# Performance work log

Measured on AMD Instinct MI355X. Metric: run time of the kernel, lower is better.

The kernel has to match this reference:

```python
import jax, jax.numpy as jnp
import numpy as np
from jax import lax

B, CIN, H, W = 8, 256, 32, 32
DK, DV, NH = 256, 256, 8
DKH = DK // NH
COUT = 512  # output_dim; conv path has COUT - DV channels
KS, PAD = 3, 1


def setup_inputs() -> dict:
    key = jax.random.key(0)
    ks = jax.random.split(key, 9)
    scale = DKH ** (-0.5)
    return {
        "x": jax.random.normal(ks[0], (B, CIN, H, W), jnp.float32),
        "w_qkv": jax.random.normal(ks[1], (2 * DK + DV, CIN), jnp.float32) * 0.02,
        "b_qkv": jnp.zeros((2 * DK + DV,), jnp.float32),
        "w_attn": jax.random.normal(ks[2], (DV, DV), jnp.float32) * 0.02,
        "b_attn": jnp.zeros((DV,), jnp.float32),
        "w_out": jax.random.normal(ks[3], (COUT - DV, CIN, KS, KS), jnp.float32) * 0.02,
        "b_out": jnp.zeros((COUT - DV,), jnp.float32),
        # original: dkh**-0.5 + torch.rand(2*W-1, dkh)
        "key_rel_w": scale + jax.random.uniform(ks[4], (2 * W - 1, DKH), jnp.float32),
        "key_rel_h": scale + jax.random.uniform(ks[5], (2 * H - 1, DKH), jnp.float32),
    }


def _conv1x1(x, w, b):
    return jnp.einsum("bchw,oc->bohw", x, w) + b[None, :, None, None]


def _rel_to_abs(x):
    # x: [b, nh, L, 2L-1] -> [b, nh, L, L] via pad-reshape-slice trick
    b, nh, L, _ = x.shape
    x = jnp.pad(x, ((0, 0), (0, 0), (0, 0), (0, 1)))            # [b,nh,L,2L]
    flat = x.reshape(b, nh, L * 2 * L)
    flat = jnp.pad(flat, ((0, 0), (0, 0), (0, L - 1)))
    final = flat.reshape(b, nh, L + 1, 2 * L - 1)
    return final[:, :, :L, L - 1:]


def _rel_logits_1d(q5, rel_k, h, w, nh, perm):
    # q5: [b, nh, dkh, h, w]; rel_k: [2w-1, dkh]
    b = q5.shape[0]
    rel = jnp.einsum("bhdxy,md->bhxym", q5, rel_k)               # [b,nh,h,w,2w-1]
    rel = rel.reshape(b, nh * h, w, 2 * w - 1)
    rel = _rel_to_abs(rel)                                        # [b,nh*h,w,w]
    rel = rel.reshape(b, nh, h, w, w)
    rel = jnp.broadcast_to(rel[:, :, :, None], (b, nh, h, h, w, w))
    rel = jnp.transpose(rel, perm)                                # [b,nh,H,W,H,W]
    return rel.reshape(b, nh, h * w, h * w)


def reference(x, w_qkv, b_qkv, w_attn, b_attn, w_out, b_out, key_rel_w, key_rel_h):
    b = x.shape[0]
    hw = H * W
    # parallel conv path (3x3, pad 1)
    conv_out = lax.conv_general_dilated(
        x, w_out, window_strides=(1, 1), padding=((PAD, PAD), (PAD, PAD)),
        dimension_numbers=("NCHW", "OIHW", "NCHW")) + b_out[None, :, None, None]
    # qkv via 1x1 conv
    qkv = _conv1x1(x, w_qkv, b_qkv)
    q, k, v = jnp.split(qkv, [DK, 2 * DK], axis=1)
    q = q.reshape(b, NH, DKH, hw) * (DKH ** (-0.5))
    k = k.reshape(b, NH, DKH, hw)
    v = v.reshape(b, NH, DV // NH, hw)
    logits = jnp.einsum("bhdq,bhdk->bhqk", q, k)                  # [b,nh,HW,HW]
    q5 = q.reshape(b, NH, DKH, H, W)
    w_rel = _rel_logits_1d(q5, key_rel_w, H, W, NH, (0, 1, 2, 4, 3, 5))
    h_rel = _rel_logits_1d(jnp.transpose(q5, (0, 1, 2, 4, 3)), key_rel_h, W, H, NH,
                           (0, 1, 4, 2, 5, 3))
    logits = logits + h_rel + w_rel
    weights = jax.nn.softmax(logits, axis=-1)
    attn = jnp.einsum("bhqk,bhdk->bhdq", weights, v)              # [b,nh,dvh,HW]
    attn = attn.reshape(b, DV, H, W)
    attn = _conv1x1(attn, w_attn, b_attn)
    return jnp.concatenate([conv_out, attn], axis=1)
```

## Files before the change

kernel.cpp:

```cpp
#include <hip/hip_runtime.h>
#include <hip/hip_bf16.h>


typedef __hip_bfloat16 bf16;
using short8 = __attribute__((ext_vector_type(8))) short;
using short4v = __attribute__((ext_vector_type(4))) short;
using f32x4 = __attribute__((ext_vector_type(4))) float;

__device__ __forceinline__ short f2bs(float f) {
  union { bf16 b; short s; } u; u.b = __float2bfloat16(f); return u.s;
}
__device__ __forceinline__ float bs2f(short s) {
  union { unsigned u; float f; } x; x.u = ((unsigned)(unsigned short)s) << 16;
  return x.f;
}

__global__ __launch_bounds__(256) void xpose(
    const float* __restrict__ X, short* __restrict__ xt,
    short* __restrict__ xb2) {
  const int b = blockIdx.x, r = blockIdx.y;
  const int tid = threadIdx.x;
  if (r == 0 || r == 33) {
    short8 z = {};
    short* dst = xt + (((size_t)b * 34 + r) * 34) * 256;
    for (int g = tid; g < 1088; g += 256) *(short8*)(dst + g * 8) = z;
    return;
  }
  __shared__ short xls[32][264];
  {
    const float* src = X + (size_t)b * 256 * 1024 + (r - 1) * 32;
    for (int it = 0; it < 8; ++it) {
      int idx = it * 256 + tid;
      int c = idx >> 3, pq = idx & 7;
      float4 f4 = *(const float4*)(src + (size_t)c * 1024 + pq * 4);
      xls[pq * 4 + 0][c] = f2bs(f4.x);
      xls[pq * 4 + 1][c] = f2bs(f4.y);
      xls[pq * 4 + 2][c] = f2bs(f4.z);
      xls[pq * 4 + 3][c] = f2bs(f4.w);
    }
  }
  __syncthreads();
  {
    short* dst = xt + (((size_t)b * 34 + r) * 34) * 256;
    for (int it = 0; it < 4; ++it) {
      int idx = it * 256 + tid;
      int cc = idx >> 5, co = idx & 31;
      short8 v = *(const short8*)&xls[cc][co * 8];
      *(short8*)(dst + (cc + 1) * 256 + co * 8) = v;
    }
    if (tid < 64) {
      short8 z = {};
      int cce = (tid >> 5) * 33, co = tid & 31;
      *(short8*)(dst + cce * 256 + co * 8) = z;
    }
  }
  {
    short* dst = xb2 + (((size_t)b * 64 + (r - 1) * 2) * 8) * 512;
    for (int it = 0; it < 4; ++it) {
      int g = it * 256 + tid;
      int half = g >> 9, c8 = (g >> 6) & 7, grp = (g >> 4) & 3, pcol = g & 15;
      short8 v = *(const short8*)&xls[half * 16 + pcol][c8 * 32 + grp * 8];
      *(short8*)(dst + ((half * 8 + c8) * 64 + grp * 16 + pcol) * 8) = v;
    }
  }
}

__global__ __launch_bounds__(256) void wpack(
    const float* __restrict__ Wc, short* __restrict__ Wb,
    const float* __restrict__ wq, short* __restrict__ Wq,
    const float* __restrict__ wa, short* __restrict__ Wa) {
  const int bid = blockIdx.x;
  const int tid = threadIdx.x;
  if (bid < 256) {
    __shared__ float ws[2304];
    const float* src = Wc + (size_t)bid * 2304;
    for (int it = 0; it < 9; ++it) ws[it * 256 + tid] = src[it * 256 + tid];
    __syncthreads();
#pragma unroll
    for (int tap = 0; tap < 9; ++tap)
      Wb[tap * 65536 + bid * 256 + tid] = f2bs(ws[tid * 9 + tap]);
  } else if (bid < 1024) {
    int idx = (bid - 256) * 256 + tid;
    Wq[idx] = f2bs(wq[idx]);
  } else {
    int idx = (bid - 1024) * 256 + tid;
    Wa[idx] = f2bs(wa[idx]);
  }
}

__global__ __launch_bounds__(256) void qkv_mfma(
    const short* __restrict__ Wq, const short* __restrict__ xb2,
    const float* __restrict__ bias,
    short* __restrict__ qsb, short* __restrict__ ksb, short* __restrict__ vtb) {
  const int tid = threadIdx.x;
  const int w = tid >> 6, lane = tid & 63;
  const int col = lane & 15, grp = lane >> 4, g8 = grp * 8;
  const int b = blockIdx.z;
  const int p0 = blockIdx.x * 64;
  const int og = blockIdx.y * 128;
  const int ob = og + w * 16;

  const short* wa0 = Wq + (size_t)(ob + col) * 256 + g8;
  const short* wa1 = wa0 + (size_t)64 * 256;
  const short* xpb = xb2 + (((size_t)b * 64 + blockIdx.x * 4) * 8) * 512 + lane * 8;

  f32x4 acc[2][4] = {};
#pragma unroll
  for (int c8 = 0; c8 < 8; ++c8) {
    const int chb = c8 * 32;
    short8 a0 = *(const short8*)(wa0 + chb);
    short8 a1 = *(const short8*)(wa1 + chb);
    short8 b0 = *(const short8*)(xpb + c8 * 512);
    short8 b1 = *(const short8*)(xpb + 4096 + c8 * 512);
    short8 b2 = *(const short8*)(xpb + 8192 + c8 * 512);
    short8 b3 = *(const short8*)(xpb + 12288 + c8 * 512);
    acc[0][0] = __builtin_amdgcn_mfma_f32_16x16x32_bf16(a0, b0, acc[0][0], 0, 0, 0);
    acc[0][1] = __builtin_amdgcn_mfma_f32_16x16x32_bf16(a0, b1, acc[0][1], 0, 0, 0);
    acc[0][2] = __builtin_amdgcn_mfma_f32_16x16x32_bf16(a0, b2, acc[0][2], 0, 0, 0);
    acc[0][3] = __builtin_amdgcn_mfma_f32_16x16x32_bf16(a0, b3, acc[0][3], 0, 0, 0);
    acc[1][0] = __builtin_amdgcn_mfma_f32_16x16x32_bf16(a1, b0, acc[1][0], 0, 0, 0);
    acc[1][1] = __builtin_amdgcn_mfma_f32_16x16x32_bf16(a1, b1, acc[1][1], 0, 0, 0);
    acc[1][2] = __builtin_amdgcn_mfma_f32_16x16x32_bf16(a1, b2, acc[1][2], 0, 0, 0);
    acc[1][3] = __builtin_amdgcn_mfma_f32_16x16x32_bf16(a1, b3, acc[1][3], 0, 0, 0);
  }

  const float qscale = 0.17677669529663687f;
#pragma unroll
  for (int j = 0; j < 2; ++j) {
    const int obase = ob + j * 64 + grp * 4;
    const int sect = obase >> 8;
    const int nh = (obase >> 5) & 7;
    const int d0 = obase & 31;
    const size_t hb = ((size_t)(b * 8 + nh)) * 1024;
    float bv[4];
#pragma unroll
    for (int r = 0; r < 4; ++r) bv[r] = bias[obase + r];
    if (sect == 0) {
#pragma unroll
      for (int pp = 0; pp < 4; ++pp) {
        const int p = p0 + pp * 16 + col;
        short4v o4;
#pragma unroll
        for (int r = 0; r < 4; ++r)
          o4[r] = f2bs((acc[j][pp][r] + bv[r]) * qscale);
        *(short4v*)&qsb[(hb + p) * 32 + d0] = o4;
      }
    } else if (sect == 1) {
#pragma unroll
      for (int pp = 0; pp < 4; ++pp) {
        const int p = p0 + pp * 16 + col;
        short4v o4;
#pragma unroll
        for (int r = 0; r < 4; ++r)
          o4[r] = f2bs(acc[j][pp][r] + bv[r]);
        *(short4v*)&ksb[(hb + p) * 32 + d0] = o4;
      }
    } else {
#pragma unroll
      for (int pp = 0; pp < 4; ++pp) {
        const int p = p0 + pp * 16 + col;
#pragma unroll
        for (int r = 0; r < 4; ++r)
          vtb[hb * 32 + (size_t)(d0 + r) * 1024 + p] = f2bs(acc[j][pp][r] + bv[r]);
      }
    }
  }
}

__global__ __launch_bounds__(256, 4) void attn_mfma(
    const short* __restrict__ qsb, const short* __restrict__ ksb,
    const short* __restrict__ vtb,
    const float* __restrict__ relw_g, const float* __restrict__ relh_g,
    short* __restrict__ amt) {
  const int tid = threadIdx.x;
  const int w = tid >> 6, lane = tid & 63;
  const int col = lane & 15, grp = lane >> 4, g8 = grp * 8;
  const int qt = blockIdx.x * 4 + w;
  const int bnh = blockIdx.y;
  const int q0 = qt * 16;
  const int i = qt >> 1;
  const int j0 = (qt & 1) * 16;

  const short* Qb = qsb + (size_t)bnh * 32768;
  const short* Kb = ksb + (size_t)bnh * 32768;
  const short* Vb = vtb + (size_t)bnh * 32768;

  __shared__ short Gh_s[4][16][68];
  __shared__ short Gw_s[4][16][68];
  __shared__ short Pt_s[4][16][40];
  __shared__ short kvb[2][4][512];

  const short* gsrc;
  int gstep;
  if (w == 0)      { gsrc = Kb + (size_t)col * 32 + g8;          gstep = 1024; }
  else if (w == 1) { gsrc = Kb + (size_t)(16 + col) * 32 + g8;   gstep = 1024; }
  else if (w == 2) { gsrc = Vb + (size_t)col * 1024 + g8;        gstep = 32;   }
  else             { gsrc = Vb + (size_t)(16 + col) * 1024 + g8; gstep = 32;   }

  short8 stg = *(const short8*)gsrc;

  short8 b_q = *(const short8*)(Qb + (q0 + col) * 32 + g8);

  {
    const float* rels[2] = {relh_g, relw_g};
#pragma unroll
    for (int tb = 0; tb < 2; ++tb) {
      const float* relg = rels[tb];
#pragma unroll
      for (int t = 0; t < 4; ++t) {
        int m = 16 * t + col;
        int mc = m > 62 ? 62 : m;
        const float* rp = relg + mc * 32 + g8;
        float4 f0 = *(const float4*)rp;
        float4 f1 = *(const float4*)(rp + 4);
        short8 ar;
        ar[0] = f2bs(f0.x); ar[1] = f2bs(f0.y);
        ar[2] = f2bs(f0.z); ar[3] = f2bs(f0.w);
        ar[4] = f2bs(f1.x); ar[5] = f2bs(f1.y);
        ar[6] = f2bs(f1.z); ar[7] = f2bs(f1.w);
        f32x4 d = __builtin_amdgcn_mfma_f32_16x16x32_bf16(
            ar, b_q, (f32x4){0.f, 0.f, 0.f, 0.f}, 0, 0, 0);
        short4v o;
        o[0] = f2bs(d[0]); o[1] = f2bs(d[1]);
        o[2] = f2bs(d[2]); o[3] = f2bs(d[3]);
        short* Gd = tb ? &Gw_s[w][0][0] : &Gh_s[w][0][0];
        *(short4v*)(Gd + col * 68 + 16 * t + grp * 4) = o;
      }
    }
  }
  __asm__ volatile("s_waitcnt lgkmcnt(0)" ::: "memory");

  float gw[8];
#pragma unroll
  for (int t = 0; t < 2; ++t)
#pragma unroll
    for (int r = 0; r < 4; ++r)
      gw[t * 4 + r] =
          bs2f(Gw_s[w][col][t * 16 + grp * 4 + r - j0 - col + 31]);

  const short8 a_one = {0x3F80, 0x3F80, 0x3F80, 0x3F80,
                        0x3F80, 0x3F80, 0x3F80, 0x3F80};

  f32x4 acc0 = {0.f, 0.f, 0.f, 0.f};
  f32x4 acc1 = {0.f, 0.f, 0.f, 0.f};
  f32x4 accl = {0.f, 0.f, 0.f, 0.f};

  *(short8*)&kvb[0][w][lane * 8] = stg;
  __syncthreads();

#pragma unroll 1
  for (int c = 0; c < 32; ++c) {
    const int cur = c & 1;
    if (c < 31) stg = *(const short8*)(gsrc + (size_t)(c + 1) * gstep);

    short8 ck0 = *(const short8*)&kvb[cur][0][lane * 8];
    short8 ck1 = *(const short8*)&kvb[cur][1][lane * 8];
    short8 cv0 = *(const short8*)&kvb[cur][2][lane * 8];
    short8 cv1 = *(const short8*)&kvb[cur][3][lane * 8];

    f32x4 s0 = __builtin_amdgcn_mfma_f32_16x16x32_bf16(
        ck0, b_q, (f32x4){0.f, 0.f, 0.f, 0.f}, 0, 0, 0);
    f32x4 s1 = __builtin_amdgcn_mfma_f32_16x16x32_bf16(
        ck1, b_q, (f32x4){0.f, 0.f, 0.f, 0.f}, 0, 0, 0);
    float gh = bs2f(Gh_s[w][col][c - i + 31]);
    short4v p0, p1;
#pragma unroll
    for (int r = 0; r < 4; ++r) p0[r] = f2bs(__expf(s0[r] + gh + gw[r]));
#pragma unroll
    for (int r = 0; r < 4; ++r) p1[r] = f2bs(__expf(s1[r] + gh + gw[4 + r]));
    *(short4v*)&Pt_s[w][col][grp * 4] = p0;
    *(short4v*)&Pt_s[w][col][16 + grp * 4] = p1;
    __asm__ volatile("s_waitcnt lgkmcnt(0)" ::: "memory");
    short8 a_p = *(const short8*)&Pt_s[w][col][g8];
    acc0 = __builtin_amdgcn_mfma_f32_16x16x32_bf16(cv0, a_p, acc0, 0, 0, 0);
    acc1 = __builtin_amdgcn_mfma_f32_16x16x32_bf16(cv1, a_p, acc1, 0, 0, 0);
    accl = __builtin_amdgcn_mfma_f32_16x16x32_bf16(a_one, a_p, accl, 0, 0, 0);

    if (c < 31) *(short8*)&kvb[cur ^ 1][w][lane * 8] = stg;
    __syncthreads();
  }

  float rn = 1.0f / accl[0];
  const int bq = bnh >> 3, nh = bnh & 7;
  short* amb = amt + ((size_t)bq * 1024 + q0 + col) * 256 + nh * 32;
  short4v o4a, o4b;
#pragma unroll
  for (int r = 0; r < 4; ++r) {
    o4a[r] = f2bs(acc0[r] * rn);
    o4b[r] = f2bs(acc1[r] * rn);
  }
  *(short4v*)&amb[grp * 4] = o4a;
  *(short4v*)&amb[16 + grp * 4] = o4b;
}

__global__ __launch_bounds__(256) void proj_mfma(
    const short* __restrict__ Wa, const short* __restrict__ amt,
    const float* __restrict__ bias, float* __restrict__ out) {
  const int tid = threadIdx.x;
  const int w = tid >> 6, lane = tid & 63;
  const int col = lane & 15, grp = lane >> 4, g8 = grp * 8;
  const int b = blockIdx.z;
  const int p0 = blockIdx.x * 64;
  const int og = blockIdx.y * 128;
  const int ob = og + w * 16;

  const short* wa0 = Wa + (size_t)(ob + col) * 256 + g8;
  const short* wa1 = wa0 + (size_t)64 * 256;
  const short* xp0 = amt + ((size_t)b * 1024 + p0 + col) * 256 + g8;
  const short* xp1 = xp0 + (size_t)16 * 256;
  const short* xp2 = xp0 + (size_t)32 * 256;
  const short* xp3 = xp0 + (size_t)48 * 256;

  f32x4 acc[2][4] = {};
#pragma unroll
  for (int c8 = 0; c8 < 8; ++c8) {
    const int chb = c8 * 32;
    short8 a0 = *(const short8*)(wa0 + chb);
    short8 a1 = *(const short8*)(wa1 + chb);
    short8 b0 = *(const short8*)(xp0 + chb);
    short8 b1 = *(const short8*)(xp1 + chb);
    short8 b2 = *(const short8*)(xp2 + chb);
    short8 b3 = *(const short8*)(xp3 + chb);
    acc[0][0] = __builtin_amdgcn_mfma_f32_16x16x32_bf16(a0, b0, acc[0][0], 0, 0, 0);
    acc[0][1] = __builtin_amdgcn_mfma_f32_16x16x32_bf16(a0, b1, acc[0][1], 0, 0, 0);
    acc[0][2] = __builtin_amdgcn_mfma_f32_16x16x32_bf16(a0, b2, acc[0][2], 0, 0, 0);
    acc[0][3] = __builtin_amdgcn_mfma_f32_16x16x32_bf16(a0, b3, acc[0][3], 0, 0, 0);
    acc[1][0] = __builtin_amdgcn_mfma_f32_16x16x32_bf16(a1, b0, acc[1][0], 0, 0, 0);
    acc[1][1] = __builtin_amdgcn_mfma_f32_16x16x32_bf16(a1, b1, acc[1][1], 0, 0, 0);
    acc[1][2] = __builtin_amdgcn_mfma_f32_16x16x32_bf16(a1, b2, acc[1][2], 0, 0, 0);
    acc[1][3] = __builtin_amdgcn_mfma_f32_16x16x32_bf16(a1, b3, acc[1][3], 0, 0, 0);
  }

#pragma unroll
  for (int j = 0; j < 2; ++j) {
    const int obase = ob + j * 64 + grp * 4;
    float bv[4];
#pragma unroll
    for (int r = 0; r < 4; ++r) bv[r] = bias[obase + r];
#pragma unroll
    for (int pp = 0; pp < 4; ++pp) {
      const int p = p0 + pp * 16 + col;
#pragma unroll
      for (int r = 0; r < 4; ++r)
        out[((size_t)b * 512 + 256 + obase + r) * 1024 + p] =
            acc[j][pp][r] + bv[r];
    }
  }
}

__global__ __launch_bounds__(256) void conv_mfma(
    const short* __restrict__ xt, const short* __restrict__ Wb,
    const float* __restrict__ bias, float* __restrict__ out) {
  const int tid = threadIdx.x;
  const int w = tid >> 6, lane = tid & 63;
  const int col = lane & 15, grp = lane >> 4, g8 = grp * 8;
  const int r0 = blockIdx.x;
  const int oh = blockIdx.y;
  const int bb = blockIdx.z;

  __shared__ short xs[3][34][264];

  {
    const short* src = xt + (((size_t)bb * 34 + r0) * 34) * 256;
    for (int g = tid; g < 3264; g += 256) {
      int row = g / 1088;
      int rem = g - row * 1088;
      int cc = rem >> 5, chg = rem & 31;
      short8 v = *(const short8*)(src + (row * 34 + cc) * 256 + chg * 8);
      *(short8*)&xs[row][cc][chg * 8] = v;
    }
  }
  __syncthreads();

  const int ob0 = oh * 128 + w * 16;
  const int ob1 = ob0 + 64;
  const short* Wa0 = Wb + (ob0 + col) * 256 + g8;
  const short* Wa1 = Wb + (ob1 + col) * 256 + g8;

  f32x4 acc00 = {0.f, 0.f, 0.f, 0.f};
  f32x4 acc01 = {0.f, 0.f, 0.f, 0.f};
  f32x4 acc10 = {0.f, 0.f, 0.f, 0.f};
  f32x4 acc11 = {0.f, 0.f, 0.f, 0.f};

#pragma unroll 1
  for (int tap = 0; tap < 9; ++tap) {
    const int u = (tap * 11) >> 5, v = tap - 3 * u;
    const short* wa0 = Wa0 + tap * 65536;
    const short* wa1 = Wa1 + tap * 65536;
    const short* xb0 = &xs[u][col + v][g8];
    const short* xb1 = &xs[u][col + 16 + v][g8];
#pragma unroll
    for (int c8 = 0; c8 < 8; ++c8) {
      const int chb = c8 * 32;
      short8 a0 = *(const short8*)(wa0 + chb);
      short8 a1 = *(const short8*)(wa1 + chb);
      short8 b0 = *(const short8*)(xb0 + chb);
      short8 b1 = *(const short8*)(xb1 + chb);
      acc00 = __builtin_amdgcn_mfma_f32_16x16x32_bf16(a0, b0, acc00, 0, 0, 0);
      acc01 = __builtin_amdgcn_mfma_f32_16x16x32_bf16(a0, b1, acc01, 0, 0, 0);
      acc10 = __builtin_amdgcn_mfma_f32_16x16x32_bf16(a1, b0, acc10, 0, 0, 0);
      acc11 = __builtin_amdgcn_mfma_f32_16x16x32_bf16(a1, b1, acc11, 0, 0, 0);
    }
  }

  float* ob = out + (size_t)bb * 512 * 1024 + r0 * 32;
#pragma unroll
  for (int r = 0; r < 4; ++r) {
    int o0 = ob0 + grp * 4 + r;
    int o1 = ob1 + grp * 4 + r;
    float bv0 = bias[o0], bv1 = bias[o1];
    ob[(size_t)o0 * 1024 + col]      = acc00[r] + bv0;
    ob[(size_t)o0 * 1024 + 16 + col] = acc01[r] + bv0;
    ob[(size_t)o1 * 1024 + col]      = acc10[r] + bv1;
    ob[(size_t)o1 * 1024 + 16 + col] = acc11[r] + bv1;
  }
}

extern "C" void kernel_launch(void* const* d_in, const int* in_sizes, int n_in,
                              void* d_out, int out_size, void* d_ws, size_t ws_size,
                              hipStream_t stream) {
  const float* x      = (const float*)d_in[0];
  const float* w_qkv  = (const float*)d_in[1];
  const float* b_qkv  = (const float*)d_in[2];
  const float* w_attn = (const float*)d_in[3];
  const float* b_attn = (const float*)d_in[4];
  const float* w_out  = (const float*)d_in[5];
  const float* b_out  = (const float*)d_in[6];
  const float* relw   = (const float*)d_in[7];
  const float* relh   = (const float*)d_in[8];
  float* out = (float*)d_out;

  short* qsb = (short*)d_ws;
  short* ksb = qsb + (size_t)2 * 1024 * 1024;
  short* vtb = ksb + (size_t)2 * 1024 * 1024;
  short* amt = (short*)((char*)d_ws + (size_t)12 * 1024 * 1024);
  short* xt  = (short*)((char*)d_ws + (size_t)16 * 1024 * 1024);
  short* xb2 = (short*)((char*)d_ws + (size_t)21 * 1024 * 1024);
  short* Wq  = (short*)((char*)d_ws + (size_t)25 * 1024 * 1024);
  short* Wa  = (short*)((char*)d_ws + (size_t)25 * 1024 * 1024 + 512 * 1024);
  short* Wb  = (short*)((char*)d_ws + (size_t)26 * 1024 * 1024);

  xpose<<<dim3(8, 34), 256, 0, stream>>>(x, xt, xb2);
  wpack<<<1280, 256, 0, stream>>>(w_out, Wb, w_qkv, Wq, w_attn, Wa);
  qkv_mfma<<<dim3(16, 6, 8), 256, 0, stream>>>(Wq, xb2, b_qkv, qsb, ksb, vtb);
  attn_mfma<<<dim3(16, 64), 256, 0, stream>>>(qsb, ksb, vtb, relw, relh, amt);
  proj_mfma<<<dim3(16, 2, 8), 256, 0, stream>>>(Wa, amt, b_attn, out);
  conv_mfma<<<dim3(32, 2, 8), 256, 0, stream>>>(xt, Wb, b_out, out);
}
```

Before: 170.3 us.

## Process two key chunks per iteration and software-pipeline PV MFMAs

The attention kernel now loads 64 keys per loop iteration (16 iterations instead of 32), halving the number of block barriers. The P·V MFMAs for the previous chunk are deferred into the next iteration so they overlap with the QK MFMAs and exp work, using double-buffered probability tiles. The Gw scratch is aliased into the P buffer to save LDS. Occupancy hint drops from 4 to 3 blocks, which adds register headroom at the cost of fewer resident waves.

New measurement: 172.6 us. Within noise of the previous version (+1.4%).

```diff
diff --git a/kernel.cpp b/kernel.cpp
--- a/kernel.cpp
+++ b/kernel.cpp
@@ -167,7 +167,7 @@
   }
 }
 
-__global__ __launch_bounds__(256, 4) void attn_mfma(
+__global__ __launch_bounds__(256, 3) void attn_mfma(
     const short* __restrict__ qsb, const short* __restrict__ ksb,
     const short* __restrict__ vtb,
     const float* __restrict__ relw_g, const float* __restrict__ relh_g,
@@ -186,18 +186,15 @@
   const short* Vb = vtb + (size_t)bnh * 32768;
 
   __shared__ short Gh_s[4][16][68];
-  __shared__ short Gw_s[4][16][68];
-  __shared__ short Pt_s[4][16][40];
-  __shared__ short kvb[2][4][512];
-
-  const short* gsrc;
-  int gstep;
-  if (w == 0)      { gsrc = Kb + (size_t)col * 32 + g8;          gstep = 1024; }
-  else if (w == 1) { gsrc = Kb + (size_t)(16 + col) * 32 + g8;   gstep = 1024; }
-  else if (w == 2) { gsrc = Vb + (size_t)col * 1024 + g8;        gstep = 32;   }
-  else             { gsrc = Vb + (size_t)(16 + col) * 1024 + g8; gstep = 32;   }
-
-  short8 stg = *(const short8*)gsrc;
+  __shared__ short kvb[2][8][512];
+  __shared__ short Pt_s[4][2][2][16][40];
+  short* Gw_w = &Pt_s[w][0][0][0][0];
+
+  const short* gK = Kb + (size_t)(w * 16 + col) * 32 + g8;
+  const short* gV = Vb + (size_t)((w & 1) * 16 + col) * 1024 + (w >> 1) * 32 + g8;
+
+  short8 stgK = *(const short8*)gK;
+  short8 stgV = *(const short8*)gV;
 
   short8 b_q = *(const short8*)(Qb + (q0 + col) * 32 + g8);
 
@@ -223,7 +220,7 @@
         short4v o;
         o[0] = f2bs(d[0]); o[1] = f2bs(d[1]);
         o[2] = f2bs(d[2]); o[3] = f2bs(d[3]);
-        short* Gd = tb ? &Gw_s[w][0][0] : &Gh_s[w][0][0];
+        short* Gd = tb ? Gw_w : &Gh_s[w][0][0];
         *(short4v*)(Gd + col * 68 + 16 * t + grp * 4) = o;
       }
     }
@@ -236,7 +233,7 @@
 #pragma unroll
     for (int r = 0; r < 4; ++r)
       gw[t * 4 + r] =
-          bs2f(Gw_s[w][col][t * 16 + grp * 4 + r - j0 - col + 31]);
+          bs2f(Gw_w[col * 68 + t * 16 + grp * 4 + r - j0 - col + 31]);
 
   const short8 a_one = {0x3F80, 0x3F80, 0x3F80, 0x3F80,
                         0x3F80, 0x3F80, 0x3F80, 0x3F80};
@@ -245,39 +242,81 @@
   f32x4 acc1 = {0.f, 0.f, 0.f, 0.f};
   f32x4 accl = {0.f, 0.f, 0.f, 0.f};
 
-  *(short8*)&kvb[0][w][lane * 8] = stg;
+  short8 cvA0p = {}, cvA1p = {}, cvB0p = {}, cvB1p = {};
+
+  *(short8*)&kvb[0][w][lane * 8] = stgK;
+  *(short8*)&kvb[0][4 + w][lane * 8] = stgV;
   __syncthreads();
 
-#pragma unroll 1
-  for (int c = 0; c < 32; ++c) {
-    const int cur = c & 1;
-    if (c < 31) stg = *(const short8*)(gsrc + (size_t)(c + 1) * gstep);
-
-    short8 ck0 = *(const short8*)&kvb[cur][0][lane * 8];
-    short8 ck1 = *(const short8*)&kvb[cur][1][lane * 8];
-    short8 cv0 = *(const short8*)&kvb[cur][2][lane * 8];
-    short8 cv1 = *(const short8*)&kvb[cur][3][lane * 8];
+#pragma unroll 2
+  for (int it = 0; it < 16; ++it) {
+    const int cur = it & 1;
+    if (it < 15) {
+      stgK = *(const short8*)(gK + (size_t)(it + 1) * 2048);
+      stgV = *(const short8*)(gV + (size_t)(it + 1) * 64);
+    }
+    short8 ck0  = *(const short8*)&kvb[cur][0][lane * 8];
+    short8 ck1  = *(const short8*)&kvb[cur][1][lane * 8];
+    short8 ck2  = *(const short8*)&kvb[cur][2][lane * 8];
+    short8 ck3  = *(const short8*)&kvb[cur][3][lane * 8];
+    short8 cva0 = *(const short8*)&kvb[cur][4][lane * 8];
+    short8 cva1 = *(const short8*)&kvb[cur][5][lane * 8];
+    short8 cvb0 = *(const short8*)&kvb[cur][6][lane * 8];
+    short8 cvb1 = *(const short8*)&kvb[cur][7][lane * 8];
 
     f32x4 s0 = __builtin_amdgcn_mfma_f32_16x16x32_bf16(
         ck0, b_q, (f32x4){0.f, 0.f, 0.f, 0.f}, 0, 0, 0);
     f32x4 s1 = __builtin_amdgcn_mfma_f32_16x16x32_bf16(
         ck1, b_q, (f32x4){0.f, 0.f, 0.f, 0.f}, 0, 0, 0);
-    float gh = bs2f(Gh_s[w][col][c - i + 31]);
-    short4v p0, p1;
-#pragma unroll
-    for (int r = 0; r < 4; ++r) p0[r] = f2bs(__expf(s0[r] + gh + gw[r]));
-#pragma unroll
-    for (int r = 0; r < 4; ++r) p1[r] = f2bs(__expf(s1[r] + gh + gw[4 + r]));
-    *(short4v*)&Pt_s[w][col][grp * 4] = p0;
-    *(short4v*)&Pt_s[w][col][16 + grp * 4] = p1;
-    __asm__ volatile("s_waitcnt lgkmcnt(0)" ::: "memory");
-    short8 a_p = *(const short8*)&Pt_s[w][col][g8];
-    acc0 = __builtin_amdgcn_mfma_f32_16x16x32_bf16(cv0, a_p, acc0, 0, 0, 0);
-    acc1 = __builtin_amdgcn_mfma_f32_16x16x32_bf16(cv1, a_p, acc1, 0, 0, 0);
-    accl = __builtin_amdgcn_mfma_f32_16x16x32_bf16(a_one, a_p, accl, 0, 0, 0);
-
-    if (c < 31) *(short8*)&kvb[cur ^ 1][w][lane * 8] = stg;
+    f32x4 s2 = __builtin_amdgcn_mfma_f32_16x16x32_bf16(
+        ck2, b_q, (f32x4){0.f, 0.f, 0.f, 0.f}, 0, 0, 0);
+    f32x4 s3 = __builtin_amdgcn_mfma_f32_16x16x32_bf16(
+        ck3, b_q, (f32x4){0.f, 0.f, 0.f, 0.f}, 0, 0, 0);
+
+    if (it > 0) {
+      short8 pA = *(const short8*)&Pt_s[w][cur ^ 1][0][col][g8];
+      short8 pB = *(const short8*)&Pt_s[w][cur ^ 1][1][col][g8];
+      acc0 = __builtin_amdgcn_mfma_f32_16x16x32_bf16(cvA0p, pA, acc0, 0, 0, 0);
+      acc0 = __builtin_amdgcn_mfma_f32_16x16x32_bf16(cvB0p, pB, acc0, 0, 0, 0);
+      acc1 = __builtin_amdgcn_mfma_f32_16x16x32_bf16(cvA1p, pA, acc1, 0, 0, 0);
+      acc1 = __builtin_amdgcn_mfma_f32_16x16x32_bf16(cvB1p, pB, acc1, 0, 0, 0);
+      accl = __builtin_amdgcn_mfma_f32_16x16x32_bf16(a_one, pA, accl, 0, 0, 0);
+      accl = __builtin_amdgcn_mfma_f32_16x16x32_bf16(a_one, pB, accl, 0, 0, 0);
+    }
+
+    float ghA = bs2f(Gh_s[w][col][2 * it - i + 31]);
+    float ghB = bs2f(Gh_s[w][col][2 * it + 1 - i + 31]);
+    short4v p0, p1, p2, p3;
+#pragma unroll
+    for (int r = 0; r < 4; ++r) p0[r] = f2bs(__expf(s0[r] + ghA + gw[r]));
+#pragma unroll
+    for (int r = 0; r < 4; ++r) p1[r] = f2bs(__expf(s1[r] + ghA + gw[4 + r]));
+#pragma unroll
+    for (int r = 0; r < 4; ++r) p2[r] = f2bs(__expf(s2[r] + ghB + gw[r]));
+#pragma unroll
+    for (int r = 0; r < 4; ++r) p3[r] = f2bs(__expf(s3[r] + ghB + gw[4 + r]));
+    *(short4v*)&Pt_s[w][cur][0][col][grp * 4] = p0;
+    *(short4v*)&Pt_s[w][cur][0][col][16 + grp * 4] = p1;
+    *(short4v*)&Pt_s[w][cur][1][col][grp * 4] = p2;
+    *(short4v*)&Pt_s[w][cur][1][col][16 + grp * 4] = p3;
+
+    if (it < 15) {
+      *(short8*)&kvb[cur ^ 1][w][lane * 8] = stgK;
+      *(short8*)&kvb[cur ^ 1][4 + w][lane * 8] = stgV;
+    }
+    cvA0p = cva0; cvA1p = cva1; cvB0p = cvb0; cvB1p = cvb1;
     __syncthreads();
+  }
+
+  {
+    short8 pA = *(const short8*)&Pt_s[w][1][0][col][g8];
+    short8 pB = *(const short8*)&Pt_s[w][1][1][col][g8];
+    acc0 = __builtin_amdgcn_mfma_f32_16x16x32_bf16(cvA0p, pA, acc0, 0, 0, 0);
+    acc0 = __builtin_amdgcn_mfma_f32_16x16x32_bf16(cvB0p, pB, acc0, 0, 0, 0);
+    acc1 = __builtin_amdgcn_mfma_f32_16x16x32_bf16(cvA1p, pA, acc1, 0, 0, 0);
+    acc1 = __builtin_amdgcn_mfma_f32_16x16x32_bf16(cvB1p, pB, acc1, 0, 0, 0);
+    accl = __builtin_amdgcn_mfma_f32_16x16x32_bf16(a_one, pA, accl, 0, 0, 0);
+    accl = __builtin_amdgcn_mfma_f32_16x16x32_bf16(a_one, pB, accl, 0, 0, 0);
   }
 
   float rn = 1.0f / accl[0];
```
